# Kernel tuning notes

Hardware: AMD Instinct MI355X
Metric: run time of the kernel (lower is better)

Reference implementation:

```python
import jax, jax.numpy as jnp
import numpy as np

HEADS = 16
DIM_HEAD = 64
MAX_FREQ = 256.0  # lucidrains RotaryEmbedding(freqs_for='pixel', max_freq=256)


def axial_freqs(H, W, dim_head):
    # per-axis rotary dim = dim_head // 2 (RotaryEmbedding(dim=head_dim//2))
    d = dim_head // 2
    base = jnp.linspace(1.0, MAX_FREQ / 2.0, d // 2) * jnp.pi  # (d/2,)

    def axis(n):
        pos = jnp.linspace(-1.0, 1.0, n)              # pixel positions
        f = pos[:, None] * base                        # (n, d/2)
        return jnp.repeat(f, 2, axis=-1)               # (n, d) interleaved pairs

    fh = jnp.broadcast_to(axis(H)[:, None, :], (H, W, d))
    fw = jnp.broadcast_to(axis(W)[None, :, :], (H, W, d))
    return jnp.concatenate([fh, fw], axis=-1)          # (H, W, dim_head)


def apply_rope(t, freqs):
    # t: (B,T,H,W,h,d); freqs: (H,W,d)
    f = freqs[:, :, None, :]                           # broadcast over heads
    x = t.reshape(t.shape[:-1] + (t.shape[-1] // 2, 2))
    x1, x2 = x[..., 0], x[..., 1]
    rot = jnp.stack([-x2, x1], axis=-1).reshape(t.shape)  # rotate_half (interleaved)
    return t * jnp.cos(f) + rot * jnp.sin(f)


def setup_inputs() -> dict:
    key = jax.random.key(0)
    k1, k2, k3 = jax.random.split(key, 3)
    B, T, H, W, D = 1, 8, 32, 32, 1024
    inner = HEADS * DIM_HEAD
    x = jax.random.normal(k1, (B, T, H, W, D), dtype=jnp.float32)
    Wqkv = jax.random.normal(k2, (D, 3 * inner), dtype=jnp.float32) * 0.02
    Wout = jax.random.normal(k3, (inner, D), dtype=jnp.float32) * 0.02
    bout = jnp.zeros((D,), dtype=jnp.float32)
    return {"x": x, "Wqkv": Wqkv, "Wout": Wout, "bout": bout}


def reference(x, Wqkv, Wout, bout):
    B, T, H, W, D = x.shape
    qkv = x @ Wqkv                                     # (B,T,H,W,3*inner)
    q, k, v = jnp.split(qkv, 3, axis=-1)
    shp = (B, T, H, W, HEADS, DIM_HEAD)
    q, k, v = q.reshape(shp), k.reshape(shp), v.reshape(shp)
    freqs = axial_freqs(H, W, DIM_HEAD)
    q = apply_rope(q, freqs)
    k = apply_rope(k, freqs)
    S = H * W
    q = q.reshape(B * T, S, HEADS, DIM_HEAD)
    k = k.reshape(B * T, S, HEADS, DIM_HEAD)
    v = v.reshape(B * T, S, HEADS, DIM_HEAD)
    scale = 1.0 / np.sqrt(DIM_HEAD).astype(np.float32)
    att = jnp.einsum('bshd,bthd->bhst', q, k) * scale  # (BT, h, S, S)
    att = jax.nn.softmax(att, axis=-1)
    o = jnp.einsum('bhst,bthd->bshd', att, v)          # (BT, S, h, d)
    o = o.reshape(B, T, H, W, HEADS * DIM_HEAD)
    return o @ Wout + bout
```

## Files before the change

kernel.cpp:

```cpp
#include <hip/hip_runtime.h>
#include <math.h>

#define DMODEL 1024
#define NQKV   3072
#define SEQ    1024
#define NH     16
#define DH     64
#define HS     (SEQ*DH)
constexpr float PI_F   = 3.14159265358979323846f;
constexpr float LOG2E  = 1.44269504088896f;

typedef _Float16 half8   __attribute__((ext_vector_type(8)));
typedef _Float16 half4   __attribute__((ext_vector_type(4)));
typedef float    floatx4 __attribute__((ext_vector_type(4)));

__device__ __forceinline__ void gload_lds16(const _Float16* g, _Float16* l) {
    __builtin_amdgcn_global_load_lds(
        (const __attribute__((address_space(1))) unsigned int*)g,
        (__attribute__((address_space(3)))       unsigned int*)l,
        16, 0, 0);
}

__global__ __launch_bounds__(256) void cvt_f16(
    const float* __restrict__ in, _Float16* __restrict__ out, int n)
{
    int i = (blockIdx.x*256 + threadIdx.x)*8;
    if (i >= n) return;
    float4 a = *(const float4*)(in + i);
    float4 b = *(const float4*)(in + i + 4);
    half8 h;
    h[0]=(_Float16)a.x; h[1]=(_Float16)a.y; h[2]=(_Float16)a.z; h[3]=(_Float16)a.w;
    h[4]=(_Float16)b.x; h[5]=(_Float16)b.y; h[6]=(_Float16)b.z; h[7]=(_Float16)b.w;
    *(half8*)(out + i) = h;
}

__global__ __launch_bounds__(256) void tr_cvt(
    const float* __restrict__ in, _Float16* __restrict__ out, int R, int C)
{
    __shared__ float T[32][33];
    const int bx = blockIdx.x, by = blockIdx.y;
    const int tx = threadIdx.x & 31, ty = threadIdx.x >> 5;
#pragma unroll
    for (int i = 0; i < 4; ++i)
        T[ty + i*8][tx] = in[(size_t)(by*32 + ty + i*8)*C + bx*32 + tx];
    __syncthreads();
#pragma unroll
    for (int i = 0; i < 4; ++i)
        out[(size_t)(bx*32 + ty + i*8)*R + by*32 + tx] = (_Float16)T[tx][ty + i*8];
}

__global__ __launch_bounds__(512) void gemm1_f16(
    const _Float16* __restrict__ A, const _Float16* __restrict__ Bt,
    _Float16* __restrict__ C, int M, int N, int K)
{
    __shared__ _Float16 As[2][2][8192] __attribute__((aligned(16)));
    __shared__ _Float16 Bs[2][2][8192] __attribute__((aligned(16)));

    const int tid  = threadIdx.x;
    const int w    = tid >> 6, lane = tid & 63, quad = lane >> 4, l = lane & 15;
    const int wm   = (w >> 2)*128, wn = (w & 3)*64;

    int bid = blockIdx.y*gridDim.x + blockIdx.x;
    const int per = (gridDim.x*gridDim.y) >> 3;
    bid = (bid & 7)*per + (bid >> 3);
    const int bx = bid % gridDim.x, by = bid / gridDim.x;
    const int m0 = by*256, n0 = bx*256;

    const int rs   = tid >> 2;
    const int csrc = (tid & 3) ^ ((tid >> 3) & 3);
    const _Float16* ga = A  + (size_t)(m0 + rs)*K + csrc*8;
    const _Float16* gb = Bt + (size_t)(n0 + rs)*K + csrc*8;
    const int swz8 = (quad ^ ((l >> 1) & 3))*8;

#define G1_STAGE_A(buf, kt, h) do { \
    gload_lds16(ga + (size_t)(kt)*64 + (h)*32,                 &As[buf][h][w*512]); \
    gload_lds16(ga + (size_t)(kt)*64 + (h)*32 + (size_t)128*K, &As[buf][h][4096 + w*512]); \
} while (0)
#define G1_STAGE_B(buf, kt, h) do { \
    gload_lds16(gb + (size_t)(kt)*64 + (h)*32,                 &Bs[buf][h][w*512]); \
    gload_lds16(gb + (size_t)(kt)*64 + (h)*32 + (size_t)128*K, &Bs[buf][h][4096 + w*512]); \
} while (0)
#define G1_RD_A(buf, h, mt) (*(half8*)&As[buf][h][(wm + (mt)*16 + l)*32 + swz8])
#define G1_RD_B(buf, h, nt) (*(half8*)&Bs[buf][h][(wn + (nt)*16 + l)*32 + swz8])

    floatx4 acc[8][4];
#pragma unroll
    for (int i = 0; i < 8; ++i)
#pragma unroll
        for (int j = 0; j < 4; ++j)
#pragma unroll
            for (int r = 0; r < 4; ++r) acc[i][j][r] = 0.f;

    G1_STAGE_A(0, 0, 0);
    G1_STAGE_B(0, 0, 0);
    G1_STAGE_A(0, 0, 1);
    G1_STAGE_B(0, 0, 1);
    asm volatile("s_waitcnt vmcnt(4)" ::: "memory");
    __builtin_amdgcn_s_barrier();
    __builtin_amdgcn_sched_barrier(0);

    const int KT = K / 64;
    for (int kt = 0; kt < KT; ++kt) {
        const int cur = kt & 1, nxt = cur ^ 1;
        const bool pf = (kt + 1 < KT);
        half8 af[4], bf[4];

#pragma unroll
        for (int mt = 0; mt < 4; ++mt) af[mt] = G1_RD_A(cur, 0, mt);
#pragma unroll
        for (int nt = 0; nt < 4; ++nt) bf[nt] = G1_RD_B(cur, 0, nt);
        if (pf) G1_STAGE_A(nxt, kt+1, 0);
        __builtin_amdgcn_s_barrier();
        asm volatile("s_waitcnt lgkmcnt(0)" ::: "memory");
        __builtin_amdgcn_sched_barrier(0);
        __builtin_amdgcn_s_setprio(1);
#pragma unroll
        for (int mt = 0; mt < 4; ++mt)
#pragma unroll
            for (int nt = 0; nt < 4; ++nt)
                acc[mt][nt] = __builtin_amdgcn_mfma_f32_16x16x32_f16(af[mt], bf[nt], acc[mt][nt], 0, 0, 0);
        __builtin_amdgcn_s_setprio(0);
        __builtin_amdgcn_s_barrier();

#pragma unroll
        for (int mt = 0; mt < 4; ++mt) af[mt] = G1_RD_A(cur, 0, mt + 4);
        if (pf) G1_STAGE_B(nxt, kt+1, 0);
        __builtin_amdgcn_s_barrier();
        asm volatile("s_waitcnt lgkmcnt(0)" ::: "memory");
        __builtin_amdgcn_sched_barrier(0);
        __builtin_amdgcn_s_setprio(1);
#pragma unroll
        for (int mt = 0; mt < 4; ++mt)
#pragma unroll
            for (int nt = 0; nt < 4; ++nt)
                acc[mt+4][nt] = __builtin_amdgcn_mfma_f32_16x16x32_f16(af[mt], bf[nt], acc[mt+4][nt], 0, 0, 0);
        __builtin_amdgcn_s_setprio(0);
        if (pf) asm volatile("s_waitcnt vmcnt(4)" ::: "memory");
        else    asm volatile("s_waitcnt vmcnt(0)" ::: "memory");
        __builtin_amdgcn_s_barrier();

#pragma unroll
        for (int mt = 0; mt < 4; ++mt) af[mt] = G1_RD_A(cur, 1, mt);
#pragma unroll
        for (int nt = 0; nt < 4; ++nt) bf[nt] = G1_RD_B(cur, 1, nt);
        if (pf) G1_STAGE_A(nxt, kt+1, 1);
        __builtin_amdgcn_s_barrier();
        asm volatile("s_waitcnt lgkmcnt(0)" ::: "memory");
        __builtin_amdgcn_sched_barrier(0);
        __builtin_amdgcn_s_setprio(1);
#pragma unroll
        for (int mt = 0; mt < 4; ++mt)
#pragma unroll
            for (int nt = 0; nt < 4; ++nt)
                acc[mt][nt] = __builtin_amdgcn_mfma_f32_16x16x32_f16(af[mt], bf[nt], acc[mt][nt], 0, 0, 0);
        __builtin_amdgcn_s_setprio(0);
        __builtin_amdgcn_s_barrier();

#pragma unroll
        for (int mt = 0; mt < 4; ++mt) af[mt] = G1_RD_A(cur, 1, mt + 4);
        if (pf) G1_STAGE_B(nxt, kt+1, 1);
        __builtin_amdgcn_s_barrier();
        asm volatile("s_waitcnt lgkmcnt(0)" ::: "memory");
        __builtin_amdgcn_sched_barrier(0);
        __builtin_amdgcn_s_setprio(1);
#pragma unroll
        for (int mt = 0; mt < 4; ++mt)
#pragma unroll
            for (int nt = 0; nt < 4; ++nt)
                acc[mt+4][nt] = __builtin_amdgcn_mfma_f32_16x16x32_f16(af[mt], bf[nt], acc[mt+4][nt], 0, 0, 0);
        __builtin_amdgcn_s_setprio(0);
        if (pf) {
            asm volatile("s_waitcnt vmcnt(4)" ::: "memory");
        }
        __builtin_amdgcn_s_barrier();
    }

#pragma unroll
    for (int mt = 0; mt < 8; ++mt)
#pragma unroll
        for (int r = 0; r < 4; ++r) {
            size_t row = m0 + wm + mt*16 + quad*4 + r;
#pragma unroll
            for (int nt = 0; nt < 4; ++nt)
                C[row*N + n0 + wn + nt*16 + l] = (_Float16)acc[mt][nt][r];
        }
#undef G1_STAGE_A
#undef G1_STAGE_B
#undef G1_RD_A
#undef G1_RD_B
}

__global__ __launch_bounds__(256) void gemm2_f16(
    const _Float16* __restrict__ A, const _Float16* __restrict__ Bt,
    const float* __restrict__ bias, float* __restrict__ C, int M, int N, int K)
{
    __shared__ _Float16 As[128*32];
    __shared__ _Float16 Bs[128*32];
    const int tid = threadIdx.x;
    const int w = tid >> 6, lane = tid & 63, quad = lane >> 4, l = lane & 15;
    const int wm = (w & 1)*64, wn = (w >> 1)*64;
    const int m0 = blockIdx.y*128, n0 = blockIdx.x*128;

    const _Float16* a0 = A  + (size_t)(m0 + w*32      + (lane>>2))*K + (lane&3)*8;
    const _Float16* a1 = A  + (size_t)(m0 + w*32 + 16 + (lane>>2))*K + (lane&3)*8;
    const _Float16* b0 = Bt + (size_t)(n0 + w*32      + (lane>>2))*K + (lane&3)*8;
    const _Float16* b1 = Bt + (size_t)(n0 + w*32 + 16 + (lane>>2))*K + (lane&3)*8;
    _Float16* lA0 = As + w*1024;
    _Float16* lA1 = As + w*1024 + 512;
    _Float16* lB0 = Bs + w*1024;
    _Float16* lB1 = Bs + w*1024 + 512;

    floatx4 acc[4][4];
#pragma unroll
    for (int i = 0; i < 4; ++i)
#pragma unroll
        for (int j = 0; j < 4; ++j)
#pragma unroll
            for (int r = 0; r < 4; ++r) acc[i][j][r] = 0.f;

    for (int k0 = 0; k0 < K; k0 += 32) {
        __syncthreads();
        gload_lds16(a0, lA0); gload_lds16(a1, lA1);
        gload_lds16(b0, lB0); gload_lds16(b1, lB1);
        a0 += 32; a1 += 32; b0 += 32; b1 += 32;
        __syncthreads();
        half8 bf[4];
#pragma unroll
        for (int nt = 0; nt < 4; ++nt)
            bf[nt] = *(half8*)&Bs[(wn + nt*16 + l)*32 + quad*8];
#pragma unroll
        for (int mt = 0; mt < 4; ++mt) {
            half8 af = *(half8*)&As[(wm + mt*16 + l)*32 + quad*8];
#pragma unroll
            for (int nt = 0; nt < 4; ++nt)
                acc[mt][nt] = __builtin_amdgcn_mfma_f32_16x16x32_f16(af, bf[nt], acc[mt][nt], 0, 0, 0);
        }
    }
#pragma unroll
    for (int mt = 0; mt < 4; ++mt)
#pragma unroll
        for (int r = 0; r < 4; ++r) {
            size_t row = m0 + wm + mt*16 + quad*4 + r;
#pragma unroll
            for (int nt = 0; nt < 4; ++nt) {
                int col = n0 + wn + nt*16 + l;
                C[row*N + col] = acc[mt][nt][r] + bias[col];
            }
        }
}

__global__ __launch_bounds__(256) void rope_scatter(
    const _Float16* __restrict__ qkv,
    _Float16* __restrict__ qw, _Float16* __restrict__ kw,
    _Float16* __restrict__ vt)
{
    const int sc = blockIdx.x;
    const int bh = blockIdx.y;
    const int bt = bh >> 4, head = bh & 15;
    const int s0 = sc*64;
    const int tid = threadIdx.x;
    const int d0 = (tid & 7)*8;

    __shared__ _Float16 T[64][80];

#pragma unroll
    for (int half = 0; half < 2; ++half) {
        const int r = (tid >> 3) + half*32;
        const int s = s0 + r;
        const _Float16* src = qkv + (size_t)(bt*SEQ + s)*NQKV + head*DH + d0;
        half8 hq = *(const half8*)(src);
        half8 hk = *(const half8*)(src + DMODEL);
        half8 hv = *(const half8*)(src + 2*DMODEL);
        float fq[8], fk[8];
#pragma unroll
        for (int j = 0; j < 8; ++j) { fq[j] = (float)hq[j]; fk[j] = (float)hk[j]; }
        const int hp = s >> 5, wp = s & 31;
        const float ph = -1.0f + hp*(2.0f/31.0f);
        const float pw = -1.0f + wp*(2.0f/31.0f);
#pragma unroll
        for (int p = 0; p < 4; ++p) {
            int pg = (d0 >> 1) + p;
            float pos = (pg < 16) ? ph : pw;
            int   gi  = (pg < 16) ? pg : (pg - 16);
            float th  = pos * ((1.0f + gi*(127.0f/15.0f)) * PI_F);
            float sn, cs;
            sincosf(th, &sn, &cs);
            float q1 = fq[2*p], q2 = fq[2*p+1];
            fq[2*p]   = q1*cs - q2*sn;
            fq[2*p+1] = q2*cs + q1*sn;
            float k1 = fk[2*p], k2 = fk[2*p+1];
            fk[2*p]   = k1*cs - k2*sn;
            fk[2*p+1] = k2*cs + k1*sn;
        }
        half8 oq, ok;
        const float qsc = 0.125f * LOG2E;
#pragma unroll
        for (int j = 0; j < 8; ++j) {
            oq[j] = (_Float16)(fq[j]*qsc);
            ok[j] = (_Float16)fk[j];
        }
        *(half8*)(qw + (size_t)bh*HS + (size_t)s*DH + d0) = oq;
        *(half8*)(kw + (size_t)bh*HS + (size_t)s*DH + d0) = ok;
#pragma unroll
        for (int j = 0; j < 8; ++j) T[d0 + j][r] = hv[j];
    }
    __syncthreads();
    const int d = tid >> 2, so = (tid & 3)*16;
    half8 v0 = *(half8*)&T[d][so];
    half8 v1 = *(half8*)&T[d][so + 8];
    _Float16* dst = vt + (size_t)bh*HS + (size_t)d*SEQ + s0 + so;
    *(half8*)dst       = v0;
    *(half8*)(dst + 8) = v1;
}

#define BC  64
#define LDH 68

__global__ __launch_bounds__(256) void attn_mfma(
    const _Float16* __restrict__ qw, const _Float16* __restrict__ kw,
    const _Float16* __restrict__ vt, _Float16* __restrict__ om)
{
    const int qc = blockIdx.x;
    const int bh = blockIdx.y;
    const int tid  = threadIdx.x;
    const int w    = tid >> 6;
    const int lane = tid & 63;
    const int quad = lane >> 4;
    const int l    = lane & 15;

    __shared__ _Float16 Ks[2][BC][LDH];
    __shared__ _Float16 Vs[2][DH][LDH];
    __shared__ _Float16 Ps[4][32][LDH];
    __shared__ float    Ls[4][32];

    const _Float16* qp = qw + (size_t)bh*HS + (size_t)(qc*128 + w*32)*DH;
    const _Float16* kp = kw + (size_t)bh*HS;
    const _Float16* vp = vt + (size_t)bh*HS;

    half8 qf[2][2];
#pragma unroll
    for (int qt = 0; qt < 2; ++qt) {
        qf[qt][0] = *(const half8*)(qp + (size_t)(qt*16 + l)*DH + quad*8);
        qf[qt][1] = *(const half8*)(qp + (size_t)(qt*16 + l)*DH + quad*8 + 32);
    }

    const int rs = tid >> 3;
    const int cs = (tid & 7)*8;

    half8 kr0 = *(const half8*)(kp + (size_t)rs*DH + cs);
    half8 kr1 = *(const half8*)(kp + (size_t)(rs+32)*DH + cs);
    half8 vr0 = *(const half8*)(vp + (size_t)rs*SEQ + cs);
    half8 vr1 = *(const half8*)(vp + (size_t)(rs+32)*SEQ + cs);
    *(half8*)&Ks[0][rs][cs]    = kr0;
    *(half8*)&Ks[0][rs+32][cs] = kr1;
    *(half8*)&Vs[0][rs][cs]    = vr0;
    *(half8*)&Vs[0][rs+32][cs] = vr1;

    floatx4 Of[2][4];
#pragma unroll
    for (int qt = 0; qt < 2; ++qt)
#pragma unroll
        for (int dt = 0; dt < 4; ++dt)
#pragma unroll
            for (int r = 0; r < 4; ++r) Of[qt][dt][r] = 0.f;
    float lsum[2] = {0.f, 0.f};

    __syncthreads();

    for (int kc = 0; kc < SEQ/BC; ++kc) {
        const int cur = kc & 1;
        if (kc < SEQ/BC - 1) {
            const _Float16* kn = kp + (size_t)(kc+1)*BC*DH;
            const _Float16* vn = vp + (size_t)(kc+1)*BC;
            kr0 = *(const half8*)(kn + (size_t)rs*DH + cs);
            kr1 = *(const half8*)(kn + (size_t)(rs+32)*DH + cs);
            vr0 = *(const half8*)(vn + (size_t)rs*SEQ + cs);
            vr1 = *(const half8*)(vn + (size_t)(rs+32)*SEQ + cs);
        }

        floatx4 Sf[2][4];
#pragma unroll
        for (int kg = 0; kg < 4; ++kg) {
            half8 af0 = *(half8*)&Ks[cur][kg*16 + l][quad*8];
            half8 af1 = *(half8*)&Ks[cur][kg*16 + l][quad*8 + 32];
#pragma unroll
            for (int qt = 0; qt < 2; ++qt) {
                floatx4 a;
#pragma unroll
                for (int r = 0; r < 4; ++r) a[r] = 0.f;
                a = __builtin_amdgcn_mfma_f32_16x16x32_f16(af0, qf[qt][0], a, 0, 0, 0);
                a = __builtin_amdgcn_mfma_f32_16x16x32_f16(af1, qf[qt][1], a, 0, 0, 0);
                Sf[qt][kg] = a;
            }
        }
#pragma unroll
        for (int qt = 0; qt < 2; ++qt)
#pragma unroll
            for (int kg = 0; kg < 4; ++kg) {
                half4 p4;
#pragma unroll
                for (int r = 0; r < 4; ++r) {
                    float p = __builtin_amdgcn_exp2f(Sf[qt][kg][r]);
                    lsum[qt] += p;
                    p4[r] = (_Float16)p;
                }
                *(half4*)&Ps[w][qt*16 + l][kg*16 + quad*4] = p4;
            }
        half8 pa[2][2];
#pragma unroll
        for (int qt = 0; qt < 2; ++qt) {
            pa[qt][0] = *(half8*)&Ps[w][qt*16 + l][quad*8];
            pa[qt][1] = *(half8*)&Ps[w][qt*16 + l][quad*8 + 32];
        }
#pragma unroll
        for (int dt = 0; dt < 4; ++dt) {
            half8 vb0 = *(half8*)&Vs[cur][dt*16 + l][quad*8];
            half8 vb1 = *(half8*)&Vs[cur][dt*16 + l][quad*8 + 32];
#pragma unroll
            for (int qt = 0; qt < 2; ++qt) {
                Of[qt][dt] = __builtin_amdgcn_mfma_f32_16x16x32_f16(pa[qt][0], vb0, Of[qt][dt], 0, 0, 0);
                Of[qt][dt] = __builtin_amdgcn_mfma_f32_16x16x32_f16(pa[qt][1], vb1, Of[qt][dt], 0, 0, 0);
            }
        }

        if (kc < SEQ/BC - 1) {
            *(half8*)&Ks[1-cur][rs][cs]    = kr0;
            *(half8*)&Ks[1-cur][rs+32][cs] = kr1;
            *(half8*)&Vs[1-cur][rs][cs]    = vr0;
            *(half8*)&Vs[1-cur][rs+32][cs] = vr1;
        }
        __syncthreads();
    }

#pragma unroll
    for (int qt = 0; qt < 2; ++qt) {
        lsum[qt] += __shfl_xor(lsum[qt], 16);
        lsum[qt] += __shfl_xor(lsum[qt], 32);
        if (quad == 0) Ls[w][qt*16 + l] = lsum[qt];
    }
    const int bt = bh >> 4, head = bh & 15;
    _Float16* opf = om + (size_t)(bt*SEQ + qc*128 + w*32)*DMODEL + head*DH;
#pragma unroll
    for (int qt = 0; qt < 2; ++qt) {
        float inv[4];
#pragma unroll
        for (int r = 0; r < 4; ++r) inv[r] = 1.0f / Ls[w][qt*16 + quad*4 + r];
#pragma unroll
        for (int dt = 0; dt < 4; ++dt)
#pragma unroll
            for (int r = 0; r < 4; ++r)
                opf[(size_t)(qt*16 + quad*4 + r)*DMODEL + dt*16 + l] =
                    (_Float16)(Of[qt][dt][r]*inv[r]);
    }
}

extern "C" void kernel_launch(void* const* d_in, const int* in_sizes, int n_in,
                              void* d_out, int out_size, void* d_ws, size_t ws_size,
                              hipStream_t stream)
{
    const float* x    = (const float*)d_in[0];
    const float* Wqkv = (const float*)d_in[1];
    const float* Wout = (const float*)d_in[2];
    const float* bout = (const float*)d_in[3];
    float* out = (float*)d_out;

    _Float16* ws   = (_Float16*)d_ws;
    _Float16* Xh   = ws;
    _Float16* Wqkt = ws + 8388608;
    _Float16* Wot  = ws + 11534336;
    _Float16* qkvt = ws + 12582912;
    _Float16* qw   = ws + 37748736;
    _Float16* kw   = ws + 46137344;
    _Float16* vt   = ws + 54525952;
    _Float16* om   = qkvt;

    hipLaunchKernelGGL(cvt_f16, dim3(4096), dim3(256), 0, stream,
                       x, Xh, 8388608);
    hipLaunchKernelGGL(tr_cvt, dim3(96, 32), dim3(256), 0, stream,
                       Wqkv, Wqkt, 1024, 3072);
    hipLaunchKernelGGL(tr_cvt, dim3(32, 32), dim3(256), 0, stream,
                       Wout, Wot, 1024, 1024);
    hipLaunchKernelGGL(gemm1_f16, dim3(12, 32), dim3(512), 0, stream,
                       Xh, Wqkt, qkvt, 8192, NQKV, DMODEL);
    hipLaunchKernelGGL(rope_scatter, dim3(16, 128), dim3(256), 0, stream,
                       qkvt, qw, kw, vt);
    hipLaunchKernelGGL(attn_mfma, dim3(8, 128), dim3(256), 0, stream,
                       qw, kw, vt, om);
    hipLaunchKernelGGL(gemm2_f16, dim3(8, 64), dim3(256), 0, stream,
                       om, Wot, bout, out, 8192, DMODEL, DMODEL);
}
```

Before: 274.9 us.

## Shrink QKV GEMM tile to 128x256 and port pipelined scheme to output GEMM

The QKV projection GEMM moves from 256x256 to 128x256 block tiles, which doubles the grid to 768 blocks, halves the accumulator registers and restructures the prefetch and wait schedule. The output projection GEMM is rewritten from a simple single-buffered 128x128 kernel into the same double-buffered, swizzled, 512-thread 128x256 pipeline. The aim is better CU occupancy and load balance for gemm1 and overlap of loads with MFMA in gemm2. The cost is lower arithmetic intensity per block in gemm1, and the hand-tuned vmcnt counts must stay correct.

```diff
diff --git a/kernel.cpp b/kernel.cpp
--- a/kernel.cpp
+++ b/kernel.cpp
@@ -53,18 +53,18 @@
     const _Float16* __restrict__ A, const _Float16* __restrict__ Bt,
     _Float16* __restrict__ C, int M, int N, int K)
 {
-    __shared__ _Float16 As[2][2][8192] __attribute__((aligned(16)));
+    __shared__ _Float16 As[2][2][4096] __attribute__((aligned(16)));
     __shared__ _Float16 Bs[2][2][8192] __attribute__((aligned(16)));
 
     const int tid  = threadIdx.x;
     const int w    = tid >> 6, lane = tid & 63, quad = lane >> 4, l = lane & 15;
-    const int wm   = (w >> 2)*128, wn = (w & 3)*64;
+    const int wm   = (w >> 2)*64, wn = (w & 3)*64;
 
     int bid = blockIdx.y*gridDim.x + blockIdx.x;
     const int per = (gridDim.x*gridDim.y) >> 3;
     bid = (bid & 7)*per + (bid >> 3);
     const int bx = bid % gridDim.x, by = bid / gridDim.x;
-    const int m0 = by*256, n0 = bx*256;
+    const int m0 = by*128, n0 = bx*256;
 
     const int rs   = tid >> 2;
     const int csrc = (tid & 3) ^ ((tid >> 3) & 3);
@@ -72,45 +72,43 @@
     const _Float16* gb = Bt + (size_t)(n0 + rs)*K + csrc*8;
     const int swz8 = (quad ^ ((l >> 1) & 3))*8;
 
-#define G1_STAGE_A(buf, kt, h) do { \
-    gload_lds16(ga + (size_t)(kt)*64 + (h)*32,                 &As[buf][h][w*512]); \
-    gload_lds16(ga + (size_t)(kt)*64 + (h)*32 + (size_t)128*K, &As[buf][h][4096 + w*512]); \
-} while (0)
-#define G1_STAGE_B(buf, kt, h) do { \
-    gload_lds16(gb + (size_t)(kt)*64 + (h)*32,                 &Bs[buf][h][w*512]); \
-    gload_lds16(gb + (size_t)(kt)*64 + (h)*32 + (size_t)128*K, &Bs[buf][h][4096 + w*512]); \
-} while (0)
-#define G1_RD_A(buf, h, mt) (*(half8*)&As[buf][h][(wm + (mt)*16 + l)*32 + swz8])
-#define G1_RD_B(buf, h, nt) (*(half8*)&Bs[buf][h][(wn + (nt)*16 + l)*32 + swz8])
-
-    floatx4 acc[8][4];
-#pragma unroll
-    for (int i = 0; i < 8; ++i)
+    floatx4 acc[4][4];
+#pragma unroll
+    for (int i = 0; i < 4; ++i)
 #pragma unroll
         for (int j = 0; j < 4; ++j)
 #pragma unroll
             for (int r = 0; r < 4; ++r) acc[i][j][r] = 0.f;
 
-    G1_STAGE_A(0, 0, 0);
-    G1_STAGE_B(0, 0, 0);
-    G1_STAGE_A(0, 0, 1);
-    G1_STAGE_B(0, 0, 1);
-    asm volatile("s_waitcnt vmcnt(4)" ::: "memory");
-    __builtin_amdgcn_s_barrier();
-    __builtin_amdgcn_sched_barrier(0);
+    gload_lds16(ga,                        &As[0][0][w*512]);
+    gload_lds16(gb,                        &Bs[0][0][w*512]);
+    gload_lds16(gb + (size_t)128*K,        &Bs[0][0][4096 + w*512]);
+    gload_lds16(ga + 32,                   &As[0][1][w*512]);
+    gload_lds16(gb + 32,                   &Bs[0][1][w*512]);
+    gload_lds16(gb + 32 + (size_t)128*K,   &Bs[0][1][4096 + w*512]);
 
     const int KT = K / 64;
     for (int kt = 0; kt < KT; ++kt) {
         const int cur = kt & 1, nxt = cur ^ 1;
         const bool pf = (kt + 1 < KT);
+        const size_t ko = (size_t)(kt + 1)*64;
         half8 af[4], bf[4];
 
-#pragma unroll
-        for (int mt = 0; mt < 4; ++mt) af[mt] = G1_RD_A(cur, 0, mt);
-#pragma unroll
-        for (int nt = 0; nt < 4; ++nt) bf[nt] = G1_RD_B(cur, 0, nt);
-        if (pf) G1_STAGE_A(nxt, kt+1, 0);
+        if (pf) gload_lds16(ga + ko, &As[nxt][0][w*512]);
+        if (pf) { asm volatile("s_waitcnt vmcnt(4)" ::: "memory"); }
+        else    { asm volatile("s_waitcnt vmcnt(3)" ::: "memory"); }
         __builtin_amdgcn_s_barrier();
+        __builtin_amdgcn_sched_barrier(0);
+#pragma unroll
+        for (int mt = 0; mt < 4; ++mt)
+            af[mt] = *(half8*)&As[cur][0][(wm + mt*16 + l)*32 + swz8];
+#pragma unroll
+        for (int nt = 0; nt < 4; ++nt)
+            bf[nt] = *(half8*)&Bs[cur][0][(wn + nt*16 + l)*32 + swz8];
+        if (pf) {
+            gload_lds16(gb + ko,                 &Bs[nxt][0][w*512]);
+            gload_lds16(gb + ko + (size_t)128*K, &Bs[nxt][0][4096 + w*512]);
+        }
         asm volatile("s_waitcnt lgkmcnt(0)" ::: "memory");
         __builtin_amdgcn_sched_barrier(0);
         __builtin_amdgcn_s_setprio(1);
@@ -120,31 +118,22 @@
             for (int nt = 0; nt < 4; ++nt)
                 acc[mt][nt] = __builtin_amdgcn_mfma_f32_16x16x32_f16(af[mt], bf[nt], acc[mt][nt], 0, 0, 0);
         __builtin_amdgcn_s_setprio(0);
+
+        if (pf) gload_lds16(ga + ko + 32, &As[nxt][1][w*512]);
+        if (pf) { asm volatile("s_waitcnt vmcnt(4)" ::: "memory"); }
+        else    { asm volatile("s_waitcnt vmcnt(0)" ::: "memory"); }
         __builtin_amdgcn_s_barrier();
-
-#pragma unroll
-        for (int mt = 0; mt < 4; ++mt) af[mt] = G1_RD_A(cur, 0, mt + 4);
-        if (pf) G1_STAGE_B(nxt, kt+1, 0);
-        __builtin_amdgcn_s_barrier();
-        asm volatile("s_waitcnt lgkmcnt(0)" ::: "memory");
-        __builtin_amdgcn_sched_barrier(0);
-        __builtin_amdgcn_s_setprio(1);
-#pragma unroll
-        for (int mt = 0; mt < 4; ++mt)
-#pragma unroll
-            for (int nt = 0; nt < 4; ++nt)
-                acc[mt+4][nt] = __builtin_amdgcn_mfma_f32_16x16x32_f16(af[mt], bf[nt], acc[mt+4][nt], 0, 0, 0);
-        __builtin_amdgcn_s_setprio(0);
-        if (pf) asm volatile("s_waitcnt vmcnt(4)" ::: "memory");
-        else    asm volatile("s_waitcnt vmcnt(0)" ::: "memory");
-        __builtin_amdgcn_s_barrier();
-
-#pragma unroll
-        for (int mt = 0; mt < 4; ++mt) af[mt] = G1_RD_A(cur, 1, mt);
-#pragma unroll
-        for (int nt = 0; nt < 4; ++nt) bf[nt] = G1_RD_B(cur, 1, nt);
-        if (pf) G1_STAGE_A(nxt, kt+1, 1);
-        __builtin_amdgcn_s_barrier();
+        __builtin_amdgcn_sched_barrier(0);
+#pragma unroll
+        for (int mt = 0; mt < 4; ++mt)
+            af[mt] = *(half8*)&As[cur][1][(wm + mt*16 + l)*32 + swz8];
+#pragma unroll
+        for (int nt = 0; nt < 4; ++nt)
+            bf[nt] = *(half8*)&Bs[cur][1][(wn + nt*16 + l)*32 + swz8];
+        if (pf) {
+            gload_lds16(gb + ko + 32,                 &Bs[nxt][1][w*512]);
+            gload_lds16(gb + ko + 32 + (size_t)128*K, &Bs[nxt][1][4096 + w*512]);
+        }
         asm volatile("s_waitcnt lgkmcnt(0)" ::: "memory");
         __builtin_amdgcn_sched_barrier(0);
         __builtin_amdgcn_s_setprio(1);
@@ -154,29 +143,10 @@
             for (int nt = 0; nt < 4; ++nt)
                 acc[mt][nt] = __builtin_amdgcn_mfma_f32_16x16x32_f16(af[mt], bf[nt], acc[mt][nt], 0, 0, 0);
         __builtin_amdgcn_s_setprio(0);
-        __builtin_amdgcn_s_barrier();
-
-#pragma unroll
-        for (int mt = 0; mt < 4; ++mt) af[mt] = G1_RD_A(cur, 1, mt + 4);
-        if (pf) G1_STAGE_B(nxt, kt+1, 1);
-        __builtin_amdgcn_s_barrier();
-        asm volatile("s_waitcnt lgkmcnt(0)" ::: "memory");
-        __builtin_amdgcn_sched_barrier(0);
-        __builtin_amdgcn_s_setprio(1);
-#pragma unroll
-        for (int mt = 0; mt < 4; ++mt)
-#pragma unroll
-            for (int nt = 0; nt < 4; ++nt)
-                acc[mt+4][nt] = __builtin_amdgcn_mfma_f32_16x16x32_f16(af[mt], bf[nt], acc[mt+4][nt], 0, 0, 0);
-        __builtin_amdgcn_s_setprio(0);
-        if (pf) {
-            asm volatile("s_waitcnt vmcnt(4)" ::: "memory");
-        }
-        __builtin_amdgcn_s_barrier();
-    }
-
-#pragma unroll
-    for (int mt = 0; mt < 8; ++mt)
+    }
+
+#pragma unroll
+    for (int mt = 0; mt < 4; ++mt)
 #pragma unroll
         for (int r = 0; r < 4; ++r) {
             size_t row = m0 + wm + mt*16 + quad*4 + r;
@@ -184,31 +154,30 @@
             for (int nt = 0; nt < 4; ++nt)
                 C[row*N + n0 + wn + nt*16 + l] = (_Float16)acc[mt][nt][r];
         }
-#undef G1_STAGE_A
-#undef G1_STAGE_B
-#undef G1_RD_A
-#undef G1_RD_B
-}
-
-__global__ __launch_bounds__(256) void gemm2_f16(
+}
+
+__global__ __launch_bounds__(512) void gemm2_f16(
     const _Float16* __restrict__ A, const _Float16* __restrict__ Bt,
     const float* __restrict__ bias, float* __restrict__ C, int M, int N, int K)
 {
-    __shared__ _Float16 As[128*32];
-    __shared__ _Float16 Bs[128*32];
-    const int tid = threadIdx.x;
-    const int w = tid >> 6, lane = tid & 63, quad = lane >> 4, l = lane & 15;
-    const int wm = (w & 1)*64, wn = (w >> 1)*64;
-    const int m0 = blockIdx.y*128, n0 = blockIdx.x*128;
-
-    const _Float16* a0 = A  + (size_t)(m0 + w*32      + (lane>>2))*K + (lane&3)*8;
-    const _Float16* a1 = A  + (size_t)(m0 + w*32 + 16 + (lane>>2))*K + (lane&3)*8;
-    const _Float16* b0 = Bt + (size_t)(n0 + w*32      + (lane>>2))*K + (lane&3)*8;
-    const _Float16* b1 = Bt + (size_t)(n0 + w*32 + 16 + (lane>>2))*K + (lane&3)*8;
-    _Float16* lA0 = As + w*1024;
-    _Float16* lA1 = As + w*1024 + 512;
-    _Float16* lB0 = Bs + w*1024;
-    _Float16* lB1 = Bs + w*1024 + 512;
+    __shared__ _Float16 As[2][2][4096] __attribute__((aligned(16)));
+    __shared__ _Float16 Bs[2][2][8192] __attribute__((aligned(16)));
+
+    const int tid  = threadIdx.x;
+    const int w    = tid >> 6, lane = tid & 63, quad = lane >> 4, l = lane & 15;
+    const int wm   = (w >> 2)*64, wn = (w & 3)*64;
+
+    int bid = blockIdx.y*gridDim.x + blockIdx.x;
+    const int per = (gridDim.x*gridDim.y) >> 3;
+    bid = (bid & 7)*per + (bid >> 3);
+    const int bx = bid % gridDim.x, by = bid / gridDim.x;
+    const int m0 = by*128, n0 = bx*256;
+
+    const int rs   = tid >> 2;
+    const int csrc = (tid & 3) ^ ((tid >> 3) & 3);
+    const _Float16* ga = A  + (size_t)(m0 + rs)*K + csrc*8;
+    const _Float16* gb = Bt + (size_t)(n0 + rs)*K + csrc*8;
+    const int swz8 = (quad ^ ((l >> 1) & 3))*8;
 
     floatx4 acc[4][4];
 #pragma unroll
@@ -218,24 +187,71 @@
 #pragma unroll
             for (int r = 0; r < 4; ++r) acc[i][j][r] = 0.f;
 
-    for (int k0 = 0; k0 < K; k0 += 32) {
-        __syncthreads();
-        gload_lds16(a0, lA0); gload_lds16(a1, lA1);
-        gload_lds16(b0, lB0); gload_lds16(b1, lB1);
-        a0 += 32; a1 += 32; b0 += 32; b1 += 32;
-        __syncthreads();
-        half8 bf[4];
+    gload_lds16(ga,                        &As[0][0][w*512]);
+    gload_lds16(gb,                        &Bs[0][0][w*512]);
+    gload_lds16(gb + (size_t)128*K,        &Bs[0][0][4096 + w*512]);
+    gload_lds16(ga + 32,                   &As[0][1][w*512]);
+    gload_lds16(gb + 32,                   &Bs[0][1][w*512]);
+    gload_lds16(gb + 32 + (size_t)128*K,   &Bs[0][1][4096 + w*512]);
+
+    const int KT = K / 64;
+    for (int kt = 0; kt < KT; ++kt) {
+        const int cur = kt & 1, nxt = cur ^ 1;
+        const bool pf = (kt + 1 < KT);
+        const size_t ko = (size_t)(kt + 1)*64;
+        half8 af[4], bf[4];
+
+        if (pf) gload_lds16(ga + ko, &As[nxt][0][w*512]);
+        if (pf) { asm volatile("s_waitcnt vmcnt(4)" ::: "memory"); }
+        else    { asm volatile("s_waitcnt vmcnt(3)" ::: "memory"); }
+        __builtin_amdgcn_s_barrier();
+        __builtin_amdgcn_sched_barrier(0);
+#pragma unroll
+        for (int mt = 0; mt < 4; ++mt)
+            af[mt] = *(half8*)&As[cur][0][(wm + mt*16 + l)*32 + swz8];
 #pragma unroll
         for (int nt = 0; nt < 4; ++nt)
-            bf[nt] = *(half8*)&Bs[(wn + nt*16 + l)*32 + quad*8];
-#pragma unroll
-        for (int mt = 0; mt < 4; ++mt) {
-            half8 af = *(half8*)&As[(wm + mt*16 + l)*32 + quad*8];
+            bf[nt] = *(half8*)&Bs[cur][0][(wn + nt*16 + l)*32 + swz8];
+        if (pf) {
+            gload_lds16(gb + ko,                 &Bs[nxt][0][w*512]);
+            gload_lds16(gb + ko + (size_t)128*K, &Bs[nxt][0][4096 + w*512]);
+        }
+        asm volatile("s_waitcnt lgkmcnt(0)" ::: "memory");
+        __builtin_amdgcn_sched_barrier(0);
+        __builtin_amdgcn_s_setprio(1);
+#pragma unroll
+        for (int mt = 0; mt < 4; ++mt)
 #pragma unroll
             for (int nt = 0; nt < 4; ++nt)
-                acc[mt][nt] = __builtin_amdgcn_mfma_f32_16x16x32_f16(af, bf[nt], acc[mt][nt], 0, 0, 0);
-        }
-    }
+                acc[mt][nt] = __builtin_amdgcn_mfma_f32_16x16x32_f16(af[mt], bf[nt], acc[mt][nt], 0, 0, 0);
+        __builtin_amdgcn_s_setprio(0);
+
+        if (pf) gload_lds16(ga + ko + 32, &As[nxt][1][w*512]);
+        if (pf) { asm volatile("s_waitcnt vmcnt(4)" ::: "memory"); }
+        else    { asm volatile("s_waitcnt vmcnt(0)" ::: "memory"); }
+        __builtin_amdgcn_s_barrier();
+        __builtin_amdgcn_sched_barrier(0);
+#pragma unroll
+        for (int mt = 0; mt < 4; ++mt)
+            af[mt] = *(half8*)&As[cur][1][(wm + mt*16 + l)*32 + swz8];
+#pragma unroll
+        for (int nt = 0; nt < 4; ++nt)
+            bf[nt] = *(half8*)&Bs[cur][1][(wn + nt*16 + l)*32 + swz8];
+        if (pf) {
+            gload_lds16(gb + ko + 32,                 &Bs[nxt][1][w*512]);
+            gload_lds16(gb + ko + 32 + (size_t)128*K, &Bs[nxt][1][4096 + w*512]);
+        }
+        asm volatile("s_waitcnt lgkmcnt(0)" ::: "memory");
+        __builtin_amdgcn_sched_barrier(0);
+        __builtin_amdgcn_s_setprio(1);
+#pragma unroll
+        for (int mt = 0; mt < 4; ++mt)
+#pragma unroll
+            for (int nt = 0; nt < 4; ++nt)
+                acc[mt][nt] = __builtin_amdgcn_mfma_f32_16x16x32_f16(af[mt], bf[nt], acc[mt][nt], 0, 0, 0);
+        __builtin_amdgcn_s_setprio(0);
+    }
+
 #pragma unroll
     for (int mt = 0; mt < 4; ++mt)
 #pragma unroll
@@ -480,12 +496,12 @@
                        Wqkv, Wqkt, 1024, 3072);
     hipLaunchKernelGGL(tr_cvt, dim3(32, 32), dim3(256), 0, stream,
                        Wout, Wot, 1024, 1024);
-    hipLaunchKernelGGL(gemm1_f16, dim3(12, 32), dim3(512), 0, stream,
+    hipLaunchKernelGGL(gemm1_f16, dim3(12, 64), dim3(512), 0, stream,
                        Xh, Wqkt, qkvt, 8192, NQKV, DMODEL);
     hipLaunchKernelGGL(rope_scatter, dim3(16, 128), dim3(256), 0, stream,
                        qkvt, qw, kw, vt);
     hipLaunchKernelGGL(attn_mfma, dim3(8, 128), dim3(256), 0, stream,
                        qw, kw, vt, om);
-    hipLaunchKernelGGL(gemm2_f16, dim3(8, 64), dim3(256), 0, stream,
+    hipLaunchKernelGGL(gemm2_f16, dim3(4, 64), dim3(512), 0, stream,
                        om, Wot, bout, out, 8192, DMODEL, DMODEL);
 }
```

Result: faster. 259.9 us (-5.5%).
